# Optimization experiments

Measured on AMD Instinct MI355X. Metric: run time of the kernel, lower is better.

## Reference

```python
import jax, jax.numpy as jnp
import numpy as np

HID, NH_FULL, K, GAMMA = 768, 12, 9, 2
HD = HID // NH_FULL            # 64
NH = NH_FULL // GAMMA          # 6
RH = HD * NH                   # 384 reduced hidden dim
OUT_HALF = HID // 2            # 384
B, S = 8, 1024


def setup_inputs() -> dict:
    key0 = jax.random.key(0)
    ks = jax.random.split(key0, 20)
    r = lambda i, shape, sc=0.02: (jax.random.normal(ks[i], shape, dtype=jnp.float32) * sc)
    inp = {
        'query': jax.random.normal(ks[0], (B, S, HID), dtype=jnp.float32),
        'mask': jnp.ones((B, 1, 1, S), dtype=jnp.int32),
        # q/k/v projections: hidden -> reduced
        'Wq': r(1, (HID, RH)), 'bq': jnp.zeros((RH,), jnp.float32),
        'Wk': r(2, (HID, RH)), 'bk': jnp.zeros((RH,), jnp.float32),
        'Wv': r(3, (HID, RH)), 'bv': jnp.zeros((RH,), jnp.float32),
        # depthwise separable conv: depthwise [HID,1,K] + pointwise [RH,HID]
        'dw_w': r(4, (HID, 1, K), 0.1), 'dw_b': jnp.zeros((HID,), jnp.float32),
        'pw_w': r(5, (RH, HID)), 'pw_b': jnp.zeros((RH,), jnp.float32),
        # self-attn output proj: reduced -> hidden//2
        'Wsa': r(6, (RH, OUT_HALF)), 'bsa': jnp.zeros((OUT_HALF,), jnp.float32),
        # dynamic kernel layer: reduced -> K*NH
        'Wdk': r(7, (RH, K * NH)), 'bdk': jnp.zeros((K * NH,), jnp.float32),
        # dynamic attn output proj: reduced -> hidden//2
        'Wda': r(8, (RH, OUT_HALF)), 'bda': jnp.zeros((OUT_HALF,), jnp.float32),
    }
    # self_attn=True requires query==key==value
    inp['key'] = inp['query']
    inp['value'] = inp['query']
    return inp


def _forward(query, key, value, mask, Wq, bq, Wk, bk, Wv, bv,
             dw_w, dw_b, pw_w, pw_b, Wsa, bsa, Wdk, bdk, Wda, bda):
    b, s, _ = query.shape
    q = query @ Wq + bq          # [B,S,RH]
    k = key @ Wk + bk
    v = value @ Wv + bv

    # ---- depthwise separable conv over key (seq axis), 'same' padding ----
    key_t = jnp.transpose(key, (0, 2, 1))  # [B,HID,S]
    dw = jax.lax.conv_general_dilated(
        key_t, dw_w, window_strides=(1,), padding=[(K // 2, K // 2)],
        feature_group_count=HID, dimension_numbers=('NCH', 'OIH', 'NCH'))
    dw = dw + dw_b[None, :, None]          # [B,HID,S]
    ks_feat = jnp.einsum('bhs,rh->bsr', dw, pw_w) + pw_b  # [B,S,RH]

    # ---- standard multi-head self-attention branch ----
    def split(x):  # [B,S,RH] -> [B,NH,S,HD]
        return x.reshape(b, s, NH, HD).transpose(0, 2, 1, 3)
    qh, kh, vh = split(q), split(k), split(v)
    scores = jnp.einsum('bhqd,bhkd->bhqk', qh, kh) / jnp.sqrt(jnp.float32(HD))
    scores = jnp.where(mask == 0, jnp.float32(-jnp.inf), scores)
    attn_wts = jax.nn.softmax(scores, axis=-1)             # [B,NH,S,S]
    attn_out = jnp.einsum('bhqk,bhkd->bhqd', attn_wts, vh)
    attn_out = attn_out.transpose(0, 2, 1, 3).reshape(b, s, RH)
    self_out = attn_out @ Wsa + bsa                         # [B,S,HID//2]

    # ---- span dynamic conv attention branch ----
    # unfold v into sliding windows: expanded[b,s,h,d,k] = v_pad[b, s+k, h*HD+d]
    v_pad = jnp.pad(v, ((0, 0), (K // 2, K // 2), (0, 0)))  # [B,S+K-1,RH]
    windows = jnp.stack([v_pad[:, i:i + s] for i in range(K)], axis=-1)  # [B,S,RH,K]
    windows = windows.reshape(b, s, NH, HD, K)
    dyn_logits = (q * ks_feat) @ Wdk + bdk                  # [B,S,K*NH]
    dyn_kernel = jax.nn.softmax(dyn_logits.reshape(b, s, NH, K), axis=-1)
    dyn_out = jnp.einsum('bshdk,bshk->bshd', windows, dyn_kernel).reshape(b, s, RH)
    dyn_out = dyn_out @ Wda + bda                           # [B,S,HID//2]

    return attn_wts, jnp.concatenate([self_out, dyn_out], axis=-1)


def reference(query, key, value, mask, Wq, bq, Wk, bk, Wv, bv,
              dw_w, dw_b, pw_w, pw_b, Wsa, bsa, Wdk, bdk, Wda, bda):
    return _forward(query, key, value, mask, Wq, bq, Wk, bk, Wv, bv,
                    dw_w, dw_b, pw_w, pw_b, Wsa, bsa, Wdk, bdk, Wda, bda)
```

## Files before the change

### kernel.cpp

```cpp
#include <hip/hip_runtime.h>
#include <math.h>

#define B 8
#define S 1024
#define HID 768
#define RH 384
#define NH 6
#define HD 64
#define KW 9
#define KNH 54
#define OUTHALF 384
#define QLD 1152
#define EXPSCALE 0.18033688f

typedef __attribute__((ext_vector_type(8))) short short8;
typedef __attribute__((ext_vector_type(4))) float f32x4;

#define SWZ(r, c) (((r) << 6) + ((c) ^ (((r) & 7) << 3)))

__device__ __forceinline__ ushort f2bf(float x) {
    unsigned u = __float_as_uint(x);
    u += 0x7FFF + ((u >> 16) & 1);
    return (ushort)(u >> 16);
}
__device__ __forceinline__ float bf2f(ushort u) {
    return __uint_as_float(((unsigned)u) << 16);
}
__device__ __forceinline__ short8 cvt8(const float* p) {
    short8 r;
    #pragma unroll
    for (int i = 0; i < 8; i++) r[i] = (short)f2bf(p[i]);
    return r;
}

__global__ __launch_bounds__(256) void cvt_dw_fused(
    const float* __restrict__ query, const float* __restrict__ dw_w,
    const float* __restrict__ dw_b, ushort* __restrict__ Xbf,
    ushort* __restrict__ dwout)
{
    int idx = blockIdx.x*256 + threadIdx.x;
    if (idx >= B*S*(HID/8)) return;
    int c0 = (idx % (HID/8))*8;
    int s  = (idx / (HID/8)) % S;
    int b  = idx / ((HID/8)*S);

    float ctr[8];
    *(float4*)&ctr[0] = *(const float4*)(query + ((size_t)b*S + s)*HID + c0);
    *(float4*)&ctr[4] = *(const float4*)(query + ((size_t)b*S + s)*HID + c0 + 4);
    *(short8*)(Xbf + ((size_t)b*S + s)*HID + c0) = cvt8(ctr);

    float acc[8];
    *(float4*)&acc[0] = *(const float4*)(dw_b + c0);
    *(float4*)&acc[4] = *(const float4*)(dw_b + c0 + 4);
    #pragma unroll
    for (int kk = 0; kk < KW; kk++) {
        int sp = s + kk - KW/2;
        if (sp >= 0 && sp < S) {
            float row[8];
            *(float4*)&row[0] = *(const float4*)(query + ((size_t)b*S + sp)*HID + c0);
            *(float4*)&row[4] = *(const float4*)(query + ((size_t)b*S + sp)*HID + c0 + 4);
            #pragma unroll
            for (int j = 0; j < 8; j++)
                acc[j] += row[j] * dw_w[(c0+j)*KW + kk];
        }
    }
    *(short8*)(dwout + ((size_t)b*S + s)*HID + c0) = cvt8(acc);
}

__global__ __launch_bounds__(256) void prep_weights(
    const float* __restrict__ Wq, const float* __restrict__ Wk, const float* __restrict__ Wv,
    const float* __restrict__ bq, const float* __restrict__ bk, const float* __restrict__ bv,
    const float* __restrict__ pw_w, const float* __restrict__ Wsa,
    const float* __restrict__ Wda, const float* __restrict__ Wdk,
    ushort* __restrict__ WqkvT, ushort* __restrict__ pw_bf,
    ushort* __restrict__ WsaT, ushort* __restrict__ WdaT, ushort* __restrict__ WdkT,
    float* __restrict__ bqkv)
{
    int i = blockIdx.x*256 + threadIdx.x;
    if (i < 884736) {
        int n = i / 768, kk = i % 768;
        int w = n / 384, nn = n % 384;
        const float* W = (w == 0) ? Wq : (w == 1) ? Wk : Wv;
        WqkvT[i] = f2bf(W[kk*384 + nn]);
        return;
    }
    i -= 884736;
    if (i < 294912) { pw_bf[i] = f2bf(pw_w[i]); return; }
    i -= 294912;
    if (i < 147456) {
        int n = i / 384, kk = i % 384;
        WsaT[i] = f2bf(Wsa[kk*384 + n]);
        return;
    }
    i -= 147456;
    if (i < 147456) {
        int n = i / 384, kk = i % 384;
        WdaT[i] = f2bf(Wda[kk*384 + n]);
        return;
    }
    i -= 147456;
    if (i < 49152) {
        int n = i / 384, kk = i % 384;
        WdkT[i] = (n < KNH) ? f2bf(Wdk[kk*KNH + n]) : (ushort)0;
        return;
    }
    i -= 49152;
    if (i < 1152) {
        bqkv[i] = (i < 384) ? bq[i] : (i < 768) ? bk[i-384] : bv[i-768];
    }
}

template<bool OUTBF>
__global__ __launch_bounds__(256) void gemm_mfma(
    const ushort* __restrict__ A, const ushort* __restrict__ Bt,
    const float* __restrict__ bias, void* __restrict__ Cout,
    int N, int Kd, int ldc)
{
    __shared__ __attribute__((aligned(16))) ushort As[128*32];
    __shared__ __attribute__((aligned(16))) ushort Bs[128*32];
    const int t = threadIdx.x;
    const int wave = t >> 6, lane = t & 63;
    const int lr = lane & 15, lg = lane >> 4;
    const int wr = wave >> 1, wc = wave & 1;
    const int bm = blockIdx.y * 128, bn = blockIdx.x * 128;

    f32x4 acc[4][4] = {};
    const int srow = t >> 1, sseg = t & 1;
    const ushort* Arow = A + (size_t)(bm + srow)*Kd + sseg*16;
    const ushort* Brow = Bt + (size_t)(bn + srow)*Kd + sseg*16;
    const int g0 = (sseg*2) ^ (srow & 3), g1 = (sseg*2 + 1) ^ (srow & 3);
    const int swz = lg ^ (lr & 3);

    short8 av0 = *(const short8*)(Arow);
    short8 av1 = *(const short8*)(Arow + 8);
    short8 bv0 = *(const short8*)(Brow);
    short8 bv1 = *(const short8*)(Brow + 8);

    for (int k0 = 0; k0 < Kd; k0 += 32) {
        __syncthreads();
        *(short8*)&As[srow*32 + g0*8] = av0;
        *(short8*)&As[srow*32 + g1*8] = av1;
        *(short8*)&Bs[srow*32 + g0*8] = bv0;
        *(short8*)&Bs[srow*32 + g1*8] = bv1;
        __syncthreads();
        if (k0 + 32 < Kd) {
            av0 = *(const short8*)(Arow + k0 + 32);
            av1 = *(const short8*)(Arow + k0 + 40);
            bv0 = *(const short8*)(Brow + k0 + 32);
            bv1 = *(const short8*)(Brow + k0 + 40);
        }
        short8 af[4], bfr[4];
        #pragma unroll
        for (int m = 0; m < 4; m++)
            af[m] = *(const short8*)&As[(wr*64 + m*16 + lr)*32 + swz*8];
        #pragma unroll
        for (int n = 0; n < 4; n++)
            bfr[n] = *(const short8*)&Bs[(wc*64 + n*16 + lr)*32 + swz*8];
        #pragma unroll
        for (int m = 0; m < 4; m++)
            #pragma unroll
            for (int n = 0; n < 4; n++)
                acc[m][n] = __builtin_amdgcn_mfma_f32_16x16x32_bf16(af[m], bfr[n], acc[m][n], 0, 0, 0);
    }

    #pragma unroll
    for (int m = 0; m < 4; m++) {
        #pragma unroll
        for (int n = 0; n < 4; n++) {
            int gcol = bn + wc*64 + n*16 + lr;
            if (gcol >= N) continue;
            float bz = bias[gcol];
            #pragma unroll
            for (int r = 0; r < 4; r++) {
                size_t grow = bm + wr*64 + m*16 + lg*4 + r;
                float val = acc[m][n][r] + bz;
                if (OUTBF) ((ushort*)Cout)[grow*ldc + gcol] = f2bf(val);
                else       ((float*)Cout)[grow*ldc + gcol] = val;
            }
        }
    }
}

template<bool OUTBF, bool DUAL>
__global__ __launch_bounds__(256) void gemm64(
    const ushort* __restrict__ A0, const ushort* __restrict__ Bt0,
    const float* __restrict__ bias0, void* __restrict__ C0,
    const ushort* __restrict__ A1, const ushort* __restrict__ Bt1,
    const float* __restrict__ bias1,
    int N, int Kd, int ldc)
{
    __shared__ __attribute__((aligned(16))) ushort As[64*32];
    __shared__ __attribute__((aligned(16))) ushort Bs[64*32];
    const ushort* A  = (DUAL && blockIdx.z) ? A1 : A0;
    const ushort* Bt = (DUAL && blockIdx.z) ? Bt1 : Bt0;
    const float* bias = (DUAL && blockIdx.z) ? bias1 : bias0;
    const int coff = (DUAL && blockIdx.z) ? OUTHALF : 0;

    const int t = threadIdx.x;
    const int wave = t >> 6, lane = t & 63;
    const int lr = lane & 15, lg = lane >> 4;
    const int wr = wave >> 1, wc = wave & 1;
    const int bm = blockIdx.y * 64, bn = blockIdx.x * 64;

    f32x4 acc[2][2] = {};
    const int srow = t >> 2, sseg = t & 3;
    const ushort* Arow = A + (size_t)(bm + srow)*Kd + sseg*8;
    const ushort* Brow = Bt + (size_t)(bn + srow)*Kd + sseg*8;
    const int gs = sseg ^ (srow & 3);
    const int swz = lg ^ (lr & 3);

    short8 av = *(const short8*)(Arow);
    short8 bv = *(const short8*)(Brow);

    for (int k0 = 0; k0 < Kd; k0 += 32) {
        __syncthreads();
        *(short8*)&As[srow*32 + gs*8] = av;
        *(short8*)&Bs[srow*32 + gs*8] = bv;
        __syncthreads();
        if (k0 + 32 < Kd) {
            av = *(const short8*)(Arow + k0 + 32);
            bv = *(const short8*)(Brow + k0 + 32);
        }
        short8 af[2], bfr[2];
        #pragma unroll
        for (int m = 0; m < 2; m++)
            af[m] = *(const short8*)&As[(wr*32 + m*16 + lr)*32 + swz*8];
        #pragma unroll
        for (int n = 0; n < 2; n++)
            bfr[n] = *(const short8*)&Bs[(wc*32 + n*16 + lr)*32 + swz*8];
        #pragma unroll
        for (int m = 0; m < 2; m++)
            #pragma unroll
            for (int n = 0; n < 2; n++)
                acc[m][n] = __builtin_amdgcn_mfma_f32_16x16x32_bf16(af[m], bfr[n], acc[m][n], 0, 0, 0);
    }

    #pragma unroll
    for (int m = 0; m < 2; m++) {
        #pragma unroll
        for (int n = 0; n < 2; n++) {
            int gcol = bn + wc*32 + n*16 + lr;
            if (gcol >= N) continue;
            float bz = bias[gcol];
            #pragma unroll
            for (int r = 0; r < 4; r++) {
                size_t grow = bm + wr*32 + m*16 + lg*4 + r;
                float val = acc[m][n][r] + bz;
                if (OUTBF) ((ushort*)C0)[grow*ldc + gcol + coff] = f2bf(val);
                else       ((float*)C0)[grow*ldc + gcol + coff] = val;
            }
        }
    }
}

__global__ __launch_bounds__(64) void gemm_qksdk(
    const ushort* __restrict__ qkv, const ushort* __restrict__ ksf,
    const ushort* __restrict__ WdkT, const float* __restrict__ bdk,
    float* __restrict__ dynlog)
{
    const int lane = threadIdx.x;
    const int lr = lane & 15, lg = lane >> 4;
    const int r0 = blockIdx.x * 16;
    const int row = r0 + lr;

    f32x4 acc[4] = {};
    for (int ks = 0; ks < RH/32; ks++) {
        int k0 = ks*32 + lg*8;
        short8 qv = *(const short8*)(qkv + (size_t)row*QLD + k0);
        short8 kv = *(const short8*)(ksf + (size_t)row*RH + k0);
        short8 afr;
        #pragma unroll
        for (int j = 0; j < 8; j++)
            afr[j] = (short)f2bf(bf2f((ushort)qv[j]) * bf2f((ushort)kv[j]));
        #pragma unroll
        for (int t4 = 0; t4 < 4; t4++) {
            short8 bfr = *(const short8*)(WdkT + (size_t)(t4*16 + lr)*RH + k0);
            acc[t4] = __builtin_amdgcn_mfma_f32_16x16x32_bf16(afr, bfr, acc[t4], 0, 0, 0);
        }
    }
    #pragma unroll
    for (int t4 = 0; t4 < 4; t4++) {
        int n = t4*16 + lr;
        if (n >= KNH) continue;
        float bz = bdk[n];
        #pragma unroll
        for (int r = 0; r < 4; r++)
            dynlog[(size_t)(r0 + lg*4 + r)*KNH + n] = acc[t4][r] + bz;
    }
}

__global__ __launch_bounds__(256) void attn_scores(
    const ushort* __restrict__ qkv, const int* __restrict__ mask,
    ushort* __restrict__ Praw, float* __restrict__ invbuf)
{
    __shared__ __attribute__((aligned(16))) ushort Ks[2][64*64];
    __shared__ __attribute__((aligned(16))) ushort Ps[4][16*64];

    const int b = blockIdx.z, h = blockIdx.y, q0 = blockIdx.x * 64;
    const int t = threadIdx.x;
    const int wave = t >> 6, lane = t & 63;
    const int lr = lane & 15, lg = lane >> 4;

    const ushort* qrow = qkv + (size_t)(b*S + q0 + wave*16 + lr)*QLD + h*HD;
    short8 aQ0 = *(const short8*)(qrow + lg*8);
    short8 aQ1 = *(const short8*)(qrow + 32 + lg*8);

    const int srow = t >> 2, sseg = t & 3;
    const int* mrow = mask + b*S;
    const ushort* krbase = qkv + RH + (size_t)(b*S + srow)*QLD + h*HD + sseg*16;
    ushort* Psw = &Ps[wave][0];
    const size_t prow0 = (size_t)(b*NH + h)*S + q0 + wave*16;

    float lsum[4] = {0.f, 0.f, 0.f, 0.f};

    {
        short8 k0v = *(const short8*)(krbase);
        short8 k1v = *(const short8*)(krbase + 8);
        *(short8*)&Ks[0][SWZ(srow, sseg*16)]     = k0v;
        *(short8*)&Ks[0][SWZ(srow, sseg*16 + 8)] = k1v;
    }
    __syncthreads();
    int cur = 0;

    for (int kc = 0; kc < S; kc += 64) {
        short8 nk0, nk1;
        if (kc + 64 < S) {
            const ushort* kr = krbase + (size_t)(kc + 64)*QLD;
            nk0 = *(const short8*)(kr);
            nk1 = *(const short8*)(kr + 8);
        }
        #pragma unroll
        for (int t4 = 0; t4 < 4; t4++) {
            short8 b0 = *(const short8*)&Ks[cur][SWZ(t4*16 + lr, lg*8)];
            short8 b1 = *(const short8*)&Ks[cur][SWZ(t4*16 + lr, 32 + lg*8)];
            f32x4 c = {0.f, 0.f, 0.f, 0.f};
            c = __builtin_amdgcn_mfma_f32_16x16x32_bf16(aQ0, b0, c, 0, 0, 0);
            c = __builtin_amdgcn_mfma_f32_16x16x32_bf16(aQ1, b1, c, 0, 0, 0);
            float add = mrow[kc + t4*16 + lr] ? 0.f : -1e30f;
            #pragma unroll
            for (int r = 0; r < 4; r++) {
                float p = exp2f(c[r]*EXPSCALE + add);
                lsum[r] += p;
                Psw[SWZ(lg*4 + r, t4*16 + lr)] = f2bf(p);
            }
        }
        {
            int row = lane & 15, seg = lane >> 4;
            short8 p0 = *(const short8*)&Psw[SWZ(row, seg*16)];
            short8 p1 = *(const short8*)&Psw[SWZ(row, seg*16 + 8)];
            ushort* gp = Praw + (prow0 + row)*S + kc + seg*16;
            *(short8*)gp       = p0;
            *(short8*)(gp + 8) = p1;
        }
        if (kc + 64 < S) {
            *(short8*)&Ks[cur^1][SWZ(srow, sseg*16)]     = nk0;
            *(short8*)&Ks[cur^1][SWZ(srow, sseg*16 + 8)] = nk1;
        }
        __syncthreads();
        cur ^= 1;
    }

    #pragma unroll
    for (int r = 0; r < 4; r++) {
        #pragma unroll
        for (int off = 1; off < 16; off <<= 1)
            lsum[r] += __shfl_xor(lsum[r], off, 16);
    }
    if (lr == 0) {
        #pragma unroll
        for (int r = 0; r < 4; r++)
            invbuf[prow0 + lg*4 + r] = 1.f / lsum[r];
    }
}

__global__ __launch_bounds__(256) void attn_pv(
    const ushort* __restrict__ qkv, const ushort* __restrict__ Praw,
    const float* __restrict__ invbuf, float* __restrict__ out0,
    ushort* __restrict__ attnbf)
{
    __shared__ __attribute__((aligned(16))) ushort Pt[2][64*64];
    __shared__ __attribute__((aligned(16))) ushort Vt[2][64*64];

    const int b = blockIdx.z, h = blockIdx.y, q0 = blockIdx.x * 64;
    const int t = threadIdx.x;
    const int wave = t >> 6, lane = t & 63;
    const int lr = lane & 15, lg = lane >> 4;
    const int srow = t >> 2, sseg = t & 3;

    const size_t rbase = (size_t)(b*NH + h)*S + q0;
    const ushort* prbase = Praw + (rbase + srow)*S + sseg*16;
    const ushort* vbase  = qkv + 2*RH + (size_t)b*S*QLD + h*HD + srow;

    const float inv_c = invbuf[rbase + wave*16 + lr];
    float inv_o[4];
    #pragma unroll
    for (int r = 0; r < 4; r++) inv_o[r] = invbuf[rbase + wave*16 + lg*4 + r];

    {
        short8 p0 = *(const short8*)(prbase);
        short8 p1 = *(const short8*)(prbase + 8);
        ushort vb[16];
        #pragma unroll
        for (int i = 0; i < 16; i++)
            vb[i] = vbase[(size_t)(sseg*16 + i)*QLD];
        *(short8*)&Pt[0][SWZ(srow, sseg*16)]     = p0;
        *(short8*)&Pt[0][SWZ(srow, sseg*16 + 8)] = p1;
        *(short8*)&Vt[0][SWZ(srow, sseg*16)]     = *(short8*)&vb[0];
        *(short8*)&Vt[0][SWZ(srow, sseg*16 + 8)] = *(short8*)&vb[8];
    }
    __syncthreads();
    int cur = 0;

    f32x4 o[4] = {};
    const size_t orow = (rbase + wave*16 + lr)*(size_t)S;

    for (int kc = 0; kc < S; kc += 64) {
        short8 np0, np1;
        ushort vb[16];
        if (kc + 64 < S) {
            np0 = *(const short8*)(prbase + kc + 64);
            np1 = *(const short8*)(prbase + kc + 72);
            const ushort* vp = vbase + (size_t)(kc + 64)*QLD;
            #pragma unroll
            for (int i = 0; i < 16; i++)
                vb[i] = vp[(size_t)(sseg*16 + i)*QLD];
        }

        #pragma unroll
        for (int kh = 0; kh < 2; kh++) {
            short8 pa = *(const short8*)&Pt[cur][SWZ(wave*16 + lr, kh*32 + lg*8)];
            float pf[8];
            #pragma unroll
            for (int j = 0; j < 8; j++) pf[j] = bf2f((ushort)pa[j]) * inv_c;
            float* op = out0 + orow + kc + kh*32 + lg*8;
            __builtin_nontemporal_store(*(f32x4*)&pf[0], (f32x4*)op);
            __builtin_nontemporal_store(*(f32x4*)&pf[4], (f32x4*)(op + 4));
            #pragma unroll
            for (int dt = 0; dt < 4; dt++) {
                short8 vv = *(const short8*)&Vt[cur][SWZ(dt*16 + lr, kh*32 + lg*8)];
                o[dt] = __builtin_amdgcn_mfma_f32_16x16x32_bf16(pa, vv, o[dt], 0, 0, 0);
            }
        }

        if (kc + 64 < S) {
            *(short8*)&Pt[cur^1][SWZ(srow, sseg*16)]     = np0;
            *(short8*)&Pt[cur^1][SWZ(srow, sseg*16 + 8)] = np1;
            *(short8*)&Vt[cur^1][SWZ(srow, sseg*16)]     = *(short8*)&vb[0];
            *(short8*)&Vt[cur^1][SWZ(srow, sseg*16 + 8)] = *(short8*)&vb[8];
        }
        __syncthreads();
        cur ^= 1;
    }

    #pragma unroll
    for (int dt = 0; dt < 4; dt++)
        #pragma unroll
        for (int r = 0; r < 4; r++)
            attnbf[(size_t)(b*S + q0 + wave*16 + lg*4 + r)*RH + h*HD + dt*16 + lr] =
                f2bf(o[dt][r] * inv_o[r]);
}

__global__ __launch_bounds__(256) void dyn_conv(
    const float* __restrict__ logits, const ushort* __restrict__ qkv,
    ushort* __restrict__ dynout)
{
    int idx = blockIdx.x*256 + threadIdx.x;
    if (idx >= B*S*(RH/4)) return;
    int r4 = (idx % (RH/4))*4;
    int s  = (idx / (RH/4)) % S;
    int b  = idx / ((RH/4)*S);
    int h  = r4 / HD;
    const float* lg = logits + ((size_t)b*S + s)*KNH + h*KW;
    float mx = lg[0];
    #pragma unroll
    for (int kk = 1; kk < KW; kk++) mx = fmaxf(mx, lg[kk]);
    float e[KW], sum = 0.f;
    #pragma unroll
    for (int kk = 0; kk < KW; kk++) { e[kk] = __expf(lg[kk]-mx); sum += e[kk]; }
    float inv = 1.f/sum;
    float acc[4] = {0.f, 0.f, 0.f, 0.f};
    const ushort* vbase = qkv + 2*RH;
    #pragma unroll
    for (int kk = 0; kk < KW; kk++) {
        int sp = s + kk - KW/2;
        if (sp >= 0 && sp < S) {
            const ushort* vp = vbase + (size_t)(b*S + sp)*QLD + r4;
            #pragma unroll
            for (int j = 0; j < 4; j++) acc[j] += bf2f(vp[j]) * e[kk];
        }
    }
    ushort4 o;
    o.x = f2bf(acc[0]*inv); o.y = f2bf(acc[1]*inv);
    o.z = f2bf(acc[2]*inv); o.w = f2bf(acc[3]*inv);
    *(ushort4*)(dynout + ((size_t)b*S + s)*RH + r4) = o;
}

extern "C" void kernel_launch(void* const* d_in, const int* in_sizes, int n_in,
                              void* d_out, int out_size, void* d_ws, size_t ws_size,
                              hipStream_t stream) {
    const float* query = (const float*)d_in[0];
    const int*   mask  = (const int*)d_in[1];
    const float* Wq    = (const float*)d_in[2];
    const float* bq    = (const float*)d_in[3];
    const float* Wk    = (const float*)d_in[4];
    const float* bk    = (const float*)d_in[5];
    const float* Wv    = (const float*)d_in[6];
    const float* bv    = (const float*)d_in[7];
    const float* dw_w  = (const float*)d_in[8];
    const float* dw_b  = (const float*)d_in[9];
    const float* pw_w  = (const float*)d_in[10];
    const float* pw_b  = (const float*)d_in[11];
    const float* Wsa   = (const float*)d_in[12];
    const float* bsa   = (const float*)d_in[13];
    const float* Wdk   = (const float*)d_in[14];
    const float* bdk   = (const float*)d_in[15];
    const float* Wda   = (const float*)d_in[16];
    const float* bda   = (const float*)d_in[17];

    float* out0 = (float*)d_out;
    float* out1 = out0 + (size_t)B*NH*S*S;

    char* wsb = (char*)d_ws;
    size_t off = 0;
    auto alloc = [&](size_t bytes) { char* p = wsb + off; off += (bytes + 255) & ~255ull; return p; };
    ushort* Xbf    = (ushort*)alloc((size_t)B*S*HID*2);
    ushort* qkvbf  = (ushort*)alloc((size_t)B*S*QLD*2);
    ushort* dwbf   = (ushort*)alloc((size_t)B*S*HID*2);
    ushort* ksf    = (ushort*)alloc((size_t)B*S*RH*2);
    ushort* attnbf = (ushort*)alloc((size_t)B*S*RH*2);
    ushort* dynbf  = (ushort*)alloc((size_t)B*S*RH*2);
    float*  dynlog = (float*) alloc((size_t)B*S*KNH*4);
    ushort* WqkvT  = (ushort*)alloc((size_t)QLD*HID*2);
    ushort* pw_bf  = (ushort*)alloc((size_t)RH*HID*2);
    ushort* WsaT   = (ushort*)alloc((size_t)RH*RH*2);
    ushort* WdaT   = (ushort*)alloc((size_t)RH*RH*2);
    ushort* WdkT   = (ushort*)alloc((size_t)128*RH*2);
    float*  bqkv   = (float*) alloc((size_t)QLD*4);
    ushort* Praw   = (ushort*)alloc((size_t)B*NH*S*S*2);
    float*  invbuf = (float*) alloc((size_t)B*NH*S*4);

    const int M = B*S;

    prep_weights<<<(1524864 + 255)/256, 256, 0, stream>>>(
        Wq, Wk, Wv, bq, bk, bv, pw_w, Wsa, Wda, Wdk,
        WqkvT, pw_bf, WsaT, WdaT, WdkT, bqkv);

    cvt_dw_fused<<<(M*(HID/8) + 255)/256, 256, 0, stream>>>(query, dw_w, dw_b, Xbf, dwbf);

    gemm_mfma<true><<<dim3(QLD/128, M/128), 256, 0, stream>>>(
        Xbf, WqkvT, bqkv, qkvbf, QLD, HID, QLD);

    gemm64<true, false><<<dim3(RH/64, M/64), 256, 0, stream>>>(
        dwbf, pw_bf, pw_b, ksf, nullptr, nullptr, nullptr, RH, HID, RH);

    attn_scores<<<dim3(S/64, NH, B), 256, 0, stream>>>(qkvbf, mask, Praw, invbuf);
    attn_pv<<<dim3(S/64, NH, B), 256, 0, stream>>>(qkvbf, Praw, invbuf, out0, attnbf);

    gemm_qksdk<<<M/16, 64, 0, stream>>>(qkvbf, ksf, WdkT, bdk, dynlog);

    dyn_conv<<<(M*(RH/4) + 255)/256, 256, 0, stream>>>(dynlog, qkvbf, dynbf);

    gemm64<false, true><<<dim3(OUTHALF/64, M/64, 2), 256, 0, stream>>>(
        attnbf, WsaT, bsa, out1, dynbf, WdaT, bda, OUTHALF, RH, HID);
}
```

Measured before the change: 299.7 us.

## Fuse prep and depthwise conv, convert fp32 in QKV GEMM, fuse dynlogits with dynconv

```diff
diff --git a/kernel.cpp b/kernel.cpp
--- a/kernel.cpp
+++ b/kernel.cpp
@@ -12,6 +12,8 @@
 #define OUTHALF 384
 #define QLD 1152
 #define EXPSCALE 0.18033688f
+#define PREP_BLOCKS 5957
+#define DW_BLOCKS 3072
 
 typedef __attribute__((ext_vector_type(8))) short short8;
 typedef __attribute__((ext_vector_type(4))) float f32x4;
@@ -33,21 +35,57 @@
     return r;
 }
 
-__global__ __launch_bounds__(256) void cvt_dw_fused(
+__global__ __launch_bounds__(256) void prep_dw(
+    const float* __restrict__ Wq, const float* __restrict__ Wk, const float* __restrict__ Wv,
+    const float* __restrict__ bq, const float* __restrict__ bk, const float* __restrict__ bv,
+    const float* __restrict__ pw_w, const float* __restrict__ Wsa,
+    const float* __restrict__ Wda, const float* __restrict__ Wdk,
+    ushort* __restrict__ WqkvT, ushort* __restrict__ pw_bf,
+    ushort* __restrict__ WsaT, ushort* __restrict__ WdaT, ushort* __restrict__ WdkT,
+    float* __restrict__ bqkv,
     const float* __restrict__ query, const float* __restrict__ dw_w,
-    const float* __restrict__ dw_b, ushort* __restrict__ Xbf,
-    ushort* __restrict__ dwout)
+    const float* __restrict__ dw_b, ushort* __restrict__ dwout)
 {
-    int idx = blockIdx.x*256 + threadIdx.x;
+    if (blockIdx.x < PREP_BLOCKS) {
+        int i = blockIdx.x*256 + threadIdx.x;
+        if (i < 884736) {
+            int n = i / 768, kk = i % 768;
+            int w = n / 384, nn = n % 384;
+            const float* W = (w == 0) ? Wq : (w == 1) ? Wk : Wv;
+            WqkvT[i] = f2bf(W[kk*384 + nn]);
+            return;
+        }
+        i -= 884736;
+        if (i < 294912) { pw_bf[i] = f2bf(pw_w[i]); return; }
+        i -= 294912;
+        if (i < 147456) {
+            int n = i / 384, kk = i % 384;
+            WsaT[i] = f2bf(Wsa[kk*384 + n]);
+            return;
+        }
+        i -= 147456;
+        if (i < 147456) {
+            int n = i / 384, kk = i % 384;
+            WdaT[i] = f2bf(Wda[kk*384 + n]);
+            return;
+        }
+        i -= 147456;
+        if (i < 49152) {
+            int n = i / 384, kk = i % 384;
+            WdkT[i] = (n < KNH) ? f2bf(Wdk[kk*KNH + n]) : (ushort)0;
+            return;
+        }
+        i -= 49152;
+        if (i < 1152) {
+            bqkv[i] = (i < 384) ? bq[i] : (i < 768) ? bk[i-384] : bv[i-768];
+        }
+        return;
+    }
+    int idx = (blockIdx.x - PREP_BLOCKS)*256 + threadIdx.x;
     if (idx >= B*S*(HID/8)) return;
     int c0 = (idx % (HID/8))*8;
     int s  = (idx / (HID/8)) % S;
     int b  = idx / ((HID/8)*S);
-
-    float ctr[8];
-    *(float4*)&ctr[0] = *(const float4*)(query + ((size_t)b*S + s)*HID + c0);
-    *(float4*)&ctr[4] = *(const float4*)(query + ((size_t)b*S + s)*HID + c0 + 4);
-    *(short8*)(Xbf + ((size_t)b*S + s)*HID + c0) = cvt8(ctr);
 
     float acc[8];
     *(float4*)&acc[0] = *(const float4*)(dw_b + c0);
@@ -67,52 +105,9 @@
     *(short8*)(dwout + ((size_t)b*S + s)*HID + c0) = cvt8(acc);
 }
 
-__global__ __launch_bounds__(256) void prep_weights(
-    const float* __restrict__ Wq, const float* __restrict__ Wk, const float* __restrict__ Wv,
-    const float* __restrict__ bq, const float* __restrict__ bk, const float* __restrict__ bv,
-    const float* __restrict__ pw_w, const float* __restrict__ Wsa,
-    const float* __restrict__ Wda, const float* __restrict__ Wdk,
-    ushort* __restrict__ WqkvT, ushort* __restrict__ pw_bf,
-    ushort* __restrict__ WsaT, ushort* __restrict__ WdaT, ushort* __restrict__ WdkT,
-    float* __restrict__ bqkv)
-{
-    int i = blockIdx.x*256 + threadIdx.x;
-    if (i < 884736) {
-        int n = i / 768, kk = i % 768;
-        int w = n / 384, nn = n % 384;
-        const float* W = (w == 0) ? Wq : (w == 1) ? Wk : Wv;
-        WqkvT[i] = f2bf(W[kk*384 + nn]);
-        return;
-    }
-    i -= 884736;
-    if (i < 294912) { pw_bf[i] = f2bf(pw_w[i]); return; }
-    i -= 294912;
-    if (i < 147456) {
-        int n = i / 384, kk = i % 384;
-        WsaT[i] = f2bf(Wsa[kk*384 + n]);
-        return;
-    }
-    i -= 147456;
-    if (i < 147456) {
-        int n = i / 384, kk = i % 384;
-        WdaT[i] = f2bf(Wda[kk*384 + n]);
-        return;
-    }
-    i -= 147456;
-    if (i < 49152) {
-        int n = i / 384, kk = i % 384;
-        WdkT[i] = (n < KNH) ? f2bf(Wdk[kk*KNH + n]) : (ushort)0;
-        return;
-    }
-    i -= 49152;
-    if (i < 1152) {
-        bqkv[i] = (i < 384) ? bq[i] : (i < 768) ? bk[i-384] : bv[i-768];
-    }
-}
-
-template<bool OUTBF>
+template<bool OUTBF, bool AF32>
 __global__ __launch_bounds__(256) void gemm_mfma(
-    const ushort* __restrict__ A, const ushort* __restrict__ Bt,
+    const void* __restrict__ Ap, const ushort* __restrict__ Bt,
     const float* __restrict__ bias, void* __restrict__ Cout,
     int N, int Kd, int ldc)
 {
@@ -126,15 +121,29 @@
 
     f32x4 acc[4][4] = {};
     const int srow = t >> 1, sseg = t & 1;
-    const ushort* Arow = A + (size_t)(bm + srow)*Kd + sseg*16;
-    const ushort* Brow = Bt + (size_t)(bn + srow)*Kd + sseg*16;
+    const float*  Arow32 = (const float*)Ap  + (size_t)(bm + srow)*Kd + sseg*16;
+    const ushort* Arow16 = (const ushort*)Ap + (size_t)(bm + srow)*Kd + sseg*16;
+    const ushort* Brow   = Bt + (size_t)(bn + srow)*Kd + sseg*16;
     const int g0 = (sseg*2) ^ (srow & 3), g1 = (sseg*2 + 1) ^ (srow & 3);
     const int swz = lg ^ (lr & 3);
 
-    short8 av0 = *(const short8*)(Arow);
-    short8 av1 = *(const short8*)(Arow + 8);
-    short8 bv0 = *(const short8*)(Brow);
-    short8 bv1 = *(const short8*)(Brow + 8);
+    short8 av0, av1, bv0, bv1;
+    auto loadA = [&](int k0) {
+        if (AF32) {
+            float tmp[16];
+            *(float4*)&tmp[0]  = *(const float4*)(Arow32 + k0);
+            *(float4*)&tmp[4]  = *(const float4*)(Arow32 + k0 + 4);
+            *(float4*)&tmp[8]  = *(const float4*)(Arow32 + k0 + 8);
+            *(float4*)&tmp[12] = *(const float4*)(Arow32 + k0 + 12);
+            av0 = cvt8(tmp); av1 = cvt8(tmp + 8);
+        } else {
+            av0 = *(const short8*)(Arow16 + k0);
+            av1 = *(const short8*)(Arow16 + k0 + 8);
+        }
+    };
+    loadA(0);
+    bv0 = *(const short8*)(Brow);
+    bv1 = *(const short8*)(Brow + 8);
 
     for (int k0 = 0; k0 < Kd; k0 += 32) {
         __syncthreads();
@@ -144,8 +153,7 @@
         *(short8*)&Bs[srow*32 + g1*8] = bv1;
         __syncthreads();
         if (k0 + 32 < Kd) {
-            av0 = *(const short8*)(Arow + k0 + 32);
-            av1 = *(const short8*)(Arow + k0 + 40);
+            loadA(k0 + 32);
             bv0 = *(const short8*)(Brow + k0 + 32);
             bv1 = *(const short8*)(Brow + k0 + 40);
         }
@@ -253,15 +261,16 @@
     }
 }
 
-__global__ __launch_bounds__(64) void gemm_qksdk(
+__global__ __launch_bounds__(256) void qksdk_dyn(
     const ushort* __restrict__ qkv, const ushort* __restrict__ ksf,
     const ushort* __restrict__ WdkT, const float* __restrict__ bdk,
-    float* __restrict__ dynlog)
+    ushort* __restrict__ dynout)
 {
-    const int lane = threadIdx.x;
+    __shared__ float Lg[64][56];
+    const int t = threadIdx.x, wave = t >> 6, lane = t & 63;
     const int lr = lane & 15, lg = lane >> 4;
-    const int r0 = blockIdx.x * 16;
-    const int row = r0 + lr;
+    const int r0 = blockIdx.x * 64;
+    const int row = r0 + wave*16 + lr;
 
     f32x4 acc[4] = {};
     for (int ks = 0; ks < RH/32; ks++) {
@@ -285,7 +294,38 @@
         float bz = bdk[n];
         #pragma unroll
         for (int r = 0; r < 4; r++)
-            dynlog[(size_t)(r0 + lg*4 + r)*KNH + n] = acc[t4][r] + bz;
+            Lg[wave*16 + lg*4 + r][n] = acc[t4][r] + bz;
+    }
+    __syncthreads();
+
+    const ushort* vbase = qkv + 2*RH;
+    for (int i = t; i < 64*96; i += 256) {
+        int rr = i / 96, g = i % 96;
+        int sg = r0 + rr;
+        int b = sg >> 10, s = sg & (S-1);
+        int r4 = g*4, h = r4 / HD;
+        const float* lgp = &Lg[rr][h*KW];
+        float mx = lgp[0];
+        #pragma unroll
+        for (int kk = 1; kk < KW; kk++) mx = fmaxf(mx, lgp[kk]);
+        float e[KW], sum = 0.f;
+        #pragma unroll
+        for (int kk = 0; kk < KW; kk++) { e[kk] = __expf(lgp[kk]-mx); sum += e[kk]; }
+        float inv = 1.f/sum;
+        float a4[4] = {0.f, 0.f, 0.f, 0.f};
+        #pragma unroll
+        for (int kk = 0; kk < KW; kk++) {
+            int sp = s + kk - KW/2;
+            if (sp >= 0 && sp < S) {
+                const ushort* vp = vbase + (size_t)(b*S + sp)*QLD + r4;
+                #pragma unroll
+                for (int j = 0; j < 4; j++) a4[j] += bf2f(vp[j]) * e[kk];
+            }
+        }
+        ushort4 o;
+        o.x = f2bf(a4[0]*inv); o.y = f2bf(a4[1]*inv);
+        o.z = f2bf(a4[2]*inv); o.w = f2bf(a4[3]*inv);
+        *(ushort4*)(dynout + (size_t)sg*RH + r4) = o;
     }
 }
 
@@ -458,41 +498,6 @@
         for (int r = 0; r < 4; r++)
             attnbf[(size_t)(b*S + q0 + wave*16 + lg*4 + r)*RH + h*HD + dt*16 + lr] =
                 f2bf(o[dt][r] * inv_o[r]);
-}
-
-__global__ __launch_bounds__(256) void dyn_conv(
-    const float* __restrict__ logits, const ushort* __restrict__ qkv,
-    ushort* __restrict__ dynout)
-{
-    int idx = blockIdx.x*256 + threadIdx.x;
-    if (idx >= B*S*(RH/4)) return;
-    int r4 = (idx % (RH/4))*4;
-    int s  = (idx / (RH/4)) % S;
-    int b  = idx / ((RH/4)*S);
-    int h  = r4 / HD;
-    const float* lg = logits + ((size_t)b*S + s)*KNH + h*KW;
-    float mx = lg[0];
-    #pragma unroll
-    for (int kk = 1; kk < KW; kk++) mx = fmaxf(mx, lg[kk]);
-    float e[KW], sum = 0.f;
-    #pragma unroll
-    for (int kk = 0; kk < KW; kk++) { e[kk] = __expf(lg[kk]-mx); sum += e[kk]; }
-    float inv = 1.f/sum;
-    float acc[4] = {0.f, 0.f, 0.f, 0.f};
-    const ushort* vbase = qkv + 2*RH;
-    #pragma unroll
-    for (int kk = 0; kk < KW; kk++) {
-        int sp = s + kk - KW/2;
-        if (sp >= 0 && sp < S) {
-            const ushort* vp = vbase + (size_t)(b*S + sp)*QLD + r4;
-            #pragma unroll
-            for (int j = 0; j < 4; j++) acc[j] += bf2f(vp[j]) * e[kk];
-        }
-    }
-    ushort4 o;
-    o.x = f2bf(acc[0]*inv); o.y = f2bf(acc[1]*inv);
-    o.z = f2bf(acc[2]*inv); o.w = f2bf(acc[3]*inv);
-    *(ushort4*)(dynout + ((size_t)b*S + s)*RH + r4) = o;
 }
 
 extern "C" void kernel_launch(void* const* d_in, const int* in_sizes, int n_in,
@@ -523,13 +528,11 @@
     char* wsb = (char*)d_ws;
     size_t off = 0;
     auto alloc = [&](size_t bytes) { char* p = wsb + off; off += (bytes + 255) & ~255ull; return p; };
-    ushort* Xbf    = (ushort*)alloc((size_t)B*S*HID*2);
     ushort* qkvbf  = (ushort*)alloc((size_t)B*S*QLD*2);
     ushort* dwbf   = (ushort*)alloc((size_t)B*S*HID*2);
     ushort* ksf    = (ushort*)alloc((size_t)B*S*RH*2);
     ushort* attnbf = (ushort*)alloc((size_t)B*S*RH*2);
     ushort* dynbf  = (ushort*)alloc((size_t)B*S*RH*2);
-    float*  dynlog = (float*) alloc((size_t)B*S*KNH*4);
     ushort* WqkvT  = (ushort*)alloc((size_t)QLD*HID*2);
     ushort* pw_bf  = (ushort*)alloc((size_t)RH*HID*2);
     ushort* WsaT   = (ushort*)alloc((size_t)RH*RH*2);
@@ -541,14 +544,13 @@
 
     const int M = B*S;
 
-    prep_weights<<<(1524864 + 255)/256, 256, 0, stream>>>(
+    prep_dw<<<PREP_BLOCKS + DW_BLOCKS, 256, 0, stream>>>(
         Wq, Wk, Wv, bq, bk, bv, pw_w, Wsa, Wda, Wdk,
-        WqkvT, pw_bf, WsaT, WdaT, WdkT, bqkv);
-
-    cvt_dw_fused<<<(M*(HID/8) + 255)/256, 256, 0, stream>>>(query, dw_w, dw_b, Xbf, dwbf);
-
-    gemm_mfma<true><<<dim3(QLD/128, M/128), 256, 0, stream>>>(
-        Xbf, WqkvT, bqkv, qkvbf, QLD, HID, QLD);
+        WqkvT, pw_bf, WsaT, WdaT, WdkT, bqkv,
+        query, dw_w, dw_b, dwbf);
+
+    gemm_mfma<true, true><<<dim3(QLD/128, M/128), 256, 0, stream>>>(
+        query, WqkvT, bqkv, qkvbf, QLD, HID, QLD);
 
     gemm64<true, false><<<dim3(RH/64, M/64), 256, 0, stream>>>(
         dwbf, pw_bf, pw_b, ksf, nullptr, nullptr, nullptr, RH, HID, RH);
@@ -556,9 +558,7 @@
     attn_scores<<<dim3(S/64, NH, B), 256, 0, stream>>>(qkvbf, mask, Praw, invbuf);
     attn_pv<<<dim3(S/64, NH, B), 256, 0, stream>>>(qkvbf, Praw, invbuf, out0, attnbf);
 
-    gemm_qksdk<<<M/16, 64, 0, stream>>>(qkvbf, ksf, WdkT, bdk, dynlog);
-
-    dyn_conv<<<(M*(RH/4) + 255)/256, 256, 0, stream>>>(dynlog, qkvbf, dynbf);
+    qksdk_dyn<<<M/64, 256, 0, stream>>>(qkvbf, ksf, WdkT, bdk, dynbf);
 
     gemm64<false, true><<<dim3(OUTHALF/64, M/64, 2), 256, 0, stream>>>(
         attnbf, WsaT, bsa, out1, dynbf, WdaT, bda, OUTHALF, RH, HID);
```

New measurement: 356.4 us. +18.9%, slower.
